# Performance work log

Hardware: AMD Instinct MI355X
Metric: run time of the kernel (lower is better)

The kernel has to match this reference:

```python
import jax, jax.numpy as jnp
import numpy as np

N = 50000   # nodes
E = 800000  # edges (avg degree 16)
D = 64      # in_feat
OUT = 64    # out_feat


def _layernorm(x, gamma, beta, eps=1e-5):
    m = jnp.mean(x, axis=-1, keepdims=True)
    v = jnp.mean((x - m) ** 2, axis=-1, keepdims=True)  # biased var, as torch LayerNorm
    return (x - m) * jax.lax.rsqrt(v + eps) * gamma + beta


def setup_inputs() -> dict:
    key = jax.random.key(0)
    ks = jax.random.split(key, 6)
    s1 = 1.0 / np.sqrt(D)
    s2 = 1.0 / np.sqrt(2 * D)
    return {
        "x": jax.random.normal(ks[0], (N, D), dtype=jnp.float32),
        "edge_index": jax.random.randint(ks[1], (2, E), 0, N, dtype=jnp.int64),
        "W1a": jax.random.normal(ks[2], (D, D), dtype=jnp.float32) * s1,
        "W1b": jax.random.normal(ks[3], (D, D), dtype=jnp.float32) * s1,
        "gamma1": jnp.ones((D,), jnp.float32),
        "beta1": jnp.zeros((D,), jnp.float32),
        "w": jnp.ones((D,), jnp.float32),
        "gamma2": jnp.ones((D,), jnp.float32),
        "beta2": jnp.zeros((D,), jnp.float32),
        "W2a": jax.random.normal(ks[4], (D, 2 * D), dtype=jnp.float32) * s2,
        "W2b": jax.random.normal(ks[5], (OUT, D), dtype=jnp.float32) * s1,
    }


def reference(x, edge_index, W1a, W1b, gamma1, beta1, w, gamma2, beta2, W2a, W2b):
    row, col = edge_index[0], edge_index[1]
    n = x.shape[0]
    # gather -> MLP1 (two bias-free linears with ReLU)
    msg = x[row]                                        # [E, D]
    msg = jax.nn.relu(msg @ W1a.T) @ W1b.T              # [E, D]
    # scatter_mean over destination nodes
    s = jax.ops.segment_sum(msg, col, num_segments=n)   # [N, D]
    cnt = jax.ops.segment_sum(jnp.ones((col.shape[0],), x.dtype), col, num_segments=n)
    agg = s / jnp.maximum(cnt, 1.0)[:, None]
    agg = _layernorm(agg, gamma1, beta1)
    # repulsion + residual + LayerNorm
    fx = _layernorm(x + (x - agg) * w, gamma2, beta2)
    # concat -> MLP2
    h = jnp.concatenate([fx, agg], axis=1)              # [N, 2D]
    return jax.nn.relu(h @ W2a.T) @ W2b.T               # [N, OUT]
```

## Files before the change

### kernel.cpp

```cpp
#include <hip/hip_runtime.h>
#include <hip/hip_bf16.h>

#define NN 50000
#define NE 800000
#define CAP 48
#define BINS 196
#define P1B 98
#define CHUNK 8164
#define MLPB 768
#define SUPT 782

typedef short v8s __attribute__((ext_vector_type(8)));
typedef float v4f __attribute__((ext_vector_type(4)));
#define MFMA16(a, b, c) __builtin_amdgcn_mfma_f32_16x16x32_bf16(a, b, c, 0, 0, 0)

__device__ __forceinline__ float bfu2f(unsigned short u) {
    union { unsigned int i; float f; } v; v.i = ((unsigned int)u) << 16; return v.f;
}
__device__ __forceinline__ unsigned short f2bf_rne(float f) {
    union { float f; unsigned int i; } v; v.f = f;
    unsigned int x = v.i;
    unsigned int r = x + 0x7fffu + ((x >> 16) & 1u);
    return (unsigned short)(r >> 16);
}
__device__ __forceinline__ v8s fragf32(const float* p) {
    float4 u = ((const float4*)p)[0];
    float4 v = ((const float4*)p)[1];
    v8s r;
    r[0] = (short)f2bf_rne(u.x); r[1] = (short)f2bf_rne(u.y);
    r[2] = (short)f2bf_rne(u.z); r[3] = (short)f2bf_rne(u.w);
    r[4] = (short)f2bf_rne(v.x); r[5] = (short)f2bf_rne(v.y);
    r[6] = (short)f2bf_rne(v.z); r[7] = (short)f2bf_rne(v.w);
    return r;
}
__device__ __forceinline__ v8s fragbf(const unsigned short* p) {
    union { uint4 u; v8s s; } t; t.u = *((const uint4*)p); return t.s;
}
__device__ __forceinline__ v4f vzero() { v4f z; z[0]=0.f; z[1]=0.f; z[2]=0.f; z[3]=0.f; return z; }

__global__ __launch_bounds__(256) void p1fat_k(const int* __restrict__ ei,
                                               const float* __restrict__ x,
                                               const float* __restrict__ W1a,
                                               const float* __restrict__ W1b,
                                               unsigned int* __restrict__ chunkbuf,
                                               unsigned short* __restrict__ histT,
                                               unsigned short* __restrict__ y) {
    __shared__ unsigned int smem[8616];
    int t = threadIdx.x;
    if (blockIdx.x < P1B) {
        unsigned int* hcnt = smem;
        unsigned int* scan = smem + BINS;
        unsigned int* data = smem + BINS + 256;
        int p = blockIdx.x;
        int e0 = p * CHUNK;
        int e1 = e0 + CHUNK; if (e1 > NE) e1 = NE;
        int ne = e1 - e0;
        bool i64 = ((ei[1] | ei[3] | ei[5] | ei[7]) == 0);
        for (int i = t; i < BINS; i += 256) hcnt[i] = 0;
        __syncthreads();
        unsigned int packed[32];
#pragma unroll
        for (int i = 0; i < 32; ++i) {
            int e = e0 + t + 256 * i;
            unsigned int pk = 0xFFFFFFFFu;
            if (e < e1) {
                int col = i64 ? ei[2 * (NE + e)] : ei[NE + e];
                int row = i64 ? ei[2 * e]        : ei[e];
                pk = ((unsigned int)col << 16) | (unsigned int)row;
                atomicAdd(&hcnt[col >> 8], 1u);
            }
            packed[i] = pk;
        }
        __syncthreads();
        scan[t] = (t < BINS) ? hcnt[t] : 0;
        __syncthreads();
        for (int off = 1; off < 256; off <<= 1) {
            unsigned int a = (t >= off) ? scan[t - off] : 0;
            __syncthreads();
            scan[t] += a;
            __syncthreads();
        }
        if (t < BINS) {
            unsigned int st = scan[t] - hcnt[t];
            scan[t] = st;
            hcnt[t] = st;
        }
        __syncthreads();
#pragma unroll
        for (int i = 0; i < 32; ++i) {
            unsigned int pk = packed[i];
            if (pk != 0xFFFFFFFFu) {
                unsigned int pos = atomicAdd(&hcnt[pk >> 24], 1u);
                data[pos] = pk;
            }
        }
        __syncthreads();
        unsigned int* cb = chunkbuf + (size_t)p * CHUNK;
        for (int i = t; i < ne; i += 256) cb[i] = data[i];
        for (int i = t; i < BINS; i += 256)
            histT[i * P1B + p] = (unsigned short)scan[i];
        return;
    }
    unsigned short* wa  = (unsigned short*)smem;
    unsigned short* wb  = wa + 64 * 72;
    unsigned short* h1s = wb + 64 * 72;
    for (int i = t; i < 64 * 64; i += 256) {
        int r = i >> 6, c = i & 63;
        wa[r * 72 + c] = f2bf_rne(W1a[i]);
        wb[r * 72 + c] = f2bf_rne(W1b[i]);
    }
    __syncthreads();
    int w = t >> 6, l = t & 63;
    int lm = l & 15, lq = l >> 4;
    for (int st = blockIdx.x - P1B; st < SUPT; st += MLPB) {
        int nb = st * 64;
        int arow = nb + w * 16 + lm;
        int arc = arow < NN ? arow : NN - 1;
        const float* xr = x + (size_t)arc * 64;
        v8s a0 = fragf32(xr + lq * 8);
        v8s a1 = fragf32(xr + 32 + lq * 8);
        v4f acc[4];
#pragma unroll
        for (int jt = 0; jt < 4; ++jt) acc[jt] = vzero();
#pragma unroll
        for (int jt = 0; jt < 4; ++jt) {
            const unsigned short* wr = &wa[(jt * 16 + lm) * 72];
            acc[jt] = MFMA16(a0, fragbf(wr + lq * 8), acc[jt]);
            acc[jt] = MFMA16(a1, fragbf(wr + 32 + lq * 8), acc[jt]);
        }
#pragma unroll
        for (int jt = 0; jt < 4; ++jt)
#pragma unroll
            for (int r = 0; r < 4; ++r)
                h1s[(w * 16 + lq * 4 + r) * 72 + jt * 16 + lm] = f2bf_rne(fmaxf(acc[jt][r], 0.0f));
        __syncthreads();
        v8s c0 = fragbf(&h1s[(w * 16 + lm) * 72 + lq * 8]);
        v8s c1 = fragbf(&h1s[(w * 16 + lm) * 72 + 32 + lq * 8]);
        v4f acc2[4];
#pragma unroll
        for (int jt = 0; jt < 4; ++jt) acc2[jt] = vzero();
#pragma unroll
        for (int jt = 0; jt < 4; ++jt) {
            const unsigned short* wr = &wb[(jt * 16 + lm) * 72];
            acc2[jt] = MFMA16(c0, fragbf(wr + lq * 8), acc2[jt]);
            acc2[jt] = MFMA16(c1, fragbf(wr + 32 + lq * 8), acc2[jt]);
        }
#pragma unroll
        for (int jt = 0; jt < 4; ++jt)
#pragma unroll
            for (int r = 0; r < 4; ++r) {
                int n = nb + w * 16 + lq * 4 + r;
                if (n < NN) y[(size_t)n * 64 + jt * 16 + lm] = f2bf_rne(acc2[jt][r]);
            }
        __syncthreads();
    }
}

__global__ __launch_bounds__(256) void p2_k(const unsigned int* __restrict__ chunkbuf,
                                            const unsigned short* __restrict__ histT,
                                            unsigned short* __restrict__ bucket1,
                                            int* __restrict__ cnt) {
    __shared__ unsigned int cl[256];
    __shared__ unsigned short dl[256 * CAP];
    __shared__ unsigned int scan[128];
    __shared__ unsigned short sstart[P1B];
    __shared__ unsigned short base[P1B];
    int t = threadIdx.x;
    int b = blockIdx.x;
    int c0 = b << 8;
    for (int i = t; i < 256; i += 256) cl[i] = 0;
    for (int i = t; i < 256 * CAP / 2; i += 256) ((unsigned int*)dl)[i] = 0;
    unsigned int len = 0;
    if (t < P1B) {
        unsigned int st = histT[b * P1B + t];
        int ne = NE - t * CHUNK; if (ne > CHUNK) ne = CHUNK;
        unsigned int en = (b == BINS - 1) ? (unsigned int)ne : histT[(b + 1) * P1B + t];
        len = en - st;
        sstart[t] = (unsigned short)st;
    }
    if (t < 128) scan[t] = (t < P1B) ? len : 0;
    __syncthreads();
    for (int off = 1; off < 128; off <<= 1) {
        unsigned int a = (t < 128 && t >= off) ? scan[t - off] : 0;
        __syncthreads();
        if (t < 128) scan[t] += a;
        __syncthreads();
    }
    if (t < P1B) base[t] = (unsigned short)(scan[t] - len);
    __syncthreads();
    int tot = (int)scan[P1B - 1];
    for (int k = t; k < tot; k += 256) {
        int lo = 0, hi = P1B - 1;
#pragma unroll
        for (int it = 0; it < 7; ++it) {
            int mid = (lo + hi + 1) >> 1;
            if ((int)base[mid] <= k) lo = mid; else hi = mid - 1;
        }
        int idx = (int)sstart[lo] + (k - (int)base[lo]);
        unsigned int d = chunkbuf[(size_t)lo * CHUNK + idx];
        int c = (int)(d >> 16) - c0;
        unsigned int slot = atomicAdd(&cl[c], 1u);
        if (slot < CAP) dl[c * CAP + slot] = (unsigned short)(d & 0xffffu);
    }
    __syncthreads();
    for (int i = t; i < 256; i += 256)
        if (c0 + i < NN) cnt[c0 + i] = (int)cl[i];
    uint4* dst = (uint4*)(bucket1 + (size_t)c0 * CAP);
    const uint4* src = (const uint4*)dl;
    for (int i = t; i < 256 * CAP / 8; i += 256) dst[i] = src[i];
}

__device__ __forceinline__ float wsum64(float v) {
#pragma unroll
    for (int o = 32; o > 0; o >>= 1) v += __shfl_xor(v, o, 64);
    return v;
}
__device__ __forceinline__ void ln_store(float s0, float s1, int tdeg, int n, int p, int j, int f0,
                                         const float* __restrict__ x,
                                         const float* __restrict__ g1, const float* __restrict__ b1,
                                         const float* __restrict__ wrep,
                                         const float* __restrict__ g2, const float* __restrict__ b2,
                                         unsigned short* __restrict__ h) {
    float inv = 1.0f / (float)(tdeg > 1 ? tdeg : 1);
    float a0 = s0 * inv, a1 = s1 * inv;
    float m = wsum64(a0 + a1) * (1.0f / 128.0f);
    float d0 = a0 - m, d1 = a1 - m;
    float var = wsum64(d0 * d0 + d1 * d1) * (1.0f / 128.0f);
    float r = rsqrtf(var + 1e-5f);
    float2 g1v = *(const float2*)(g1 + f0);
    float2 b1v = *(const float2*)(b1 + f0);
    a0 = d0 * r * g1v.x + b1v.x;
    a1 = d1 * r * g1v.y + b1v.y;
    float2 xv = *(const float2*)(x + (size_t)n * 64 + f0);
    float2 wv = *(const float2*)(wrep + f0);
    float t0 = xv.x + (xv.x - a0) * wv.x;
    float t1 = xv.y + (xv.y - a1) * wv.y;
    float m2 = wsum64(t0 + t1) * (1.0f / 128.0f);
    float e0 = t0 - m2, e1 = t1 - m2;
    float var2 = wsum64(e0 * e0 + e1 * e1) * (1.0f / 128.0f);
    float r2 = rsqrtf(var2 + 1e-5f);
    float2 g2v = *(const float2*)(g2 + f0);
    float2 b2v = *(const float2*)(b2 + f0);
    float fx0 = e0 * r2 * g2v.x + b2v.x;
    float fx1 = e1 * r2 * g2v.y + b2v.y;
    unsigned* hw = (unsigned*)(h + (size_t)n * 128);
    if (p == 0) hw[j]      = (unsigned)f2bf_rne(fx0) | ((unsigned)f2bf_rne(fx1) << 16);
    else        hw[32 + j] = (unsigned)f2bf_rne(a0)  | ((unsigned)f2bf_rne(a1)  << 16);
}
__global__ __launch_bounds__(256) void gathernorm_k(const int* __restrict__ cnt,
                                                    const unsigned short* __restrict__ bucket1,
                                                    const unsigned short* __restrict__ y,
                                                    const float* __restrict__ x,
                                                    const float* __restrict__ g1, const float* __restrict__ b1,
                                                    const float* __restrict__ wrep,
                                                    const float* __restrict__ g2, const float* __restrict__ b2,
                                                    unsigned short* __restrict__ h) {
    int n0 = blockIdx.x * 8 + (threadIdx.x >> 6) * 2;
    if (n0 >= NN) return;
    int n1 = n0 + 1;
    int n1c = n1 < NN ? n1 : n0;
    int l = threadIdx.x & 63;
    int p = l >> 5;
    int j = l & 31;
    int f0 = 2 * j;
    int dA = cnt[n0], dB = cnt[n1c];
    int eA = dA < CAP ? dA : CAP;
    int eB = dB < CAP ? dB : CAP;
    const uint4* bpA = (const uint4*)(bucket1 + (size_t)n0 * CAP);
    const uint4* bpB = (const uint4*)(bucket1 + (size_t)n1c * CAP);
    uint4 qA[6], qB[6];
#pragma unroll
    for (int i = 0; i < 6; ++i) { qA[i] = bpA[i]; qB[i] = bpB[i]; }
    float sA0 = 0.f, sA1 = 0.f, sB0 = 0.f, sB1 = 0.f;
#pragma unroll
    for (int c = 0; c < 6; ++c) {
        bool cA = c * 8 < eA, cB = c * 8 < eB;
        if (cA | cB) {
            unsigned wA[4] = { qA[c].x, qA[c].y, qA[c].z, qA[c].w };
            unsigned wB[4] = { qB[c].x, qB[c].y, qB[c].z, qB[c].w };
#pragma unroll
            for (int i = 0; i < 4; ++i) {
                int e = c * 8 + 2 * i + p;
                int idA = (int)((wA[i] >> (p * 16)) & 0xffffu);
                int idB = (int)((wB[i] >> (p * 16)) & 0xffffu);
                unsigned uA = *(const unsigned*)(y + (size_t)idA * 64 + f0);
                unsigned uB = *(const unsigned*)(y + (size_t)idB * 64 + f0);
                bool okA = cA && e < eA, okB = cB && e < eB;
                sA0 += okA ? bfu2f((unsigned short)(uA & 0xffffu)) : 0.0f;
                sA1 += okA ? bfu2f((unsigned short)(uA >> 16)) : 0.0f;
                sB0 += okB ? bfu2f((unsigned short)(uB & 0xffffu)) : 0.0f;
                sB1 += okB ? bfu2f((unsigned short)(uB >> 16)) : 0.0f;
            }
        }
    }
    sA0 += __shfl_xor(sA0, 32, 64);
    sA1 += __shfl_xor(sA1, 32, 64);
    sB0 += __shfl_xor(sB0, 32, 64);
    sB1 += __shfl_xor(sB1, 32, 64);
    ln_store(sA0, sA1, dA, n0, p, j, f0, x, g1, b1, wrep, g2, b2, h);
    if (n1 < NN)
        ln_store(sB0, sB1, dB, n1, p, j, f0, x, g1, b1, wrep, g2, b2, h);
}

__global__ __launch_bounds__(256) void mlp2_k(const unsigned short* hin,
                                              const float* __restrict__ W2a,
                                              const float* __restrict__ W2b,
                                              float* out) {
    __shared__ unsigned short sm2[64 * 136 + 64 * 72 + 64 * 72];
    unsigned short* wa2 = sm2;
    unsigned short* wb2 = wa2 + 64 * 136;
    unsigned short* t2s = wb2 + 64 * 72;
    int t = threadIdx.x;
    for (int i = t; i < 64 * 128; i += 256) {
        int r = i >> 7, c = i & 127;
        wa2[r * 136 + c] = f2bf_rne(W2a[i]);
    }
    for (int i = t; i < 64 * 64; i += 256) {
        int r = i >> 6, c = i & 63;
        wb2[r * 72 + c] = f2bf_rne(W2b[i]);
    }
    __syncthreads();
    int w = t >> 6, l = t & 63;
    int lm = l & 15, lq = l >> 4;
    for (int st = blockIdx.x; st < SUPT; st += MLPB) {
        int nb = st * 64;
        int arow = nb + w * 16 + lm;
        int arc = arow < NN ? arow : NN - 1;
        const unsigned short* fr = hin + (size_t)arc * 128;
        v8s a0 = fragbf(fr + lq * 8);
        v8s a1 = fragbf(fr + 32 + lq * 8);
        v8s a2 = fragbf(fr + 64 + lq * 8);
        v8s a3 = fragbf(fr + 96 + lq * 8);
        v4f acc[4];
#pragma unroll
        for (int jt = 0; jt < 4; ++jt) acc[jt] = vzero();
#pragma unroll
        for (int jt = 0; jt < 4; ++jt) {
            const unsigned short* wr = &wa2[(jt * 16 + lm) * 136];
            acc[jt] = MFMA16(a0, fragbf(wr + lq * 8), acc[jt]);
            acc[jt] = MFMA16(a1, fragbf(wr + 32 + lq * 8), acc[jt]);
            acc[jt] = MFMA16(a2, fragbf(wr + 64 + lq * 8), acc[jt]);
            acc[jt] = MFMA16(a3, fragbf(wr + 96 + lq * 8), acc[jt]);
        }
#pragma unroll
        for (int jt = 0; jt < 4; ++jt)
#pragma unroll
            for (int r = 0; r < 4; ++r)
                t2s[(w * 16 + lq * 4 + r) * 72 + jt * 16 + lm] = f2bf_rne(fmaxf(acc[jt][r], 0.0f));
        __syncthreads();
        v8s c0 = fragbf(&t2s[(w * 16 + lm) * 72 + lq * 8]);
        v8s c1 = fragbf(&t2s[(w * 16 + lm) * 72 + 32 + lq * 8]);
        v4f acc2[4];
#pragma unroll
        for (int jt = 0; jt < 4; ++jt) acc2[jt] = vzero();
#pragma unroll
        for (int jt = 0; jt < 4; ++jt) {
            const unsigned short* wr = &wb2[(jt * 16 + lm) * 72];
            acc2[jt] = MFMA16(c0, fragbf(wr + lq * 8), acc2[jt]);
            acc2[jt] = MFMA16(c1, fragbf(wr + 32 + lq * 8), acc2[jt]);
        }
#pragma unroll
        for (int jt = 0; jt < 4; ++jt)
#pragma unroll
            for (int r = 0; r < 4; ++r) {
                int n = nb + w * 16 + lq * 4 + r;
                if (n < NN) out[(size_t)n * 64 + jt * 16 + lm] = acc2[jt][r];
            }
        __syncthreads();
    }
}

extern "C" void kernel_launch(void* const* d_in, const int* in_sizes, int n_in,
                              void* d_out, int out_size, void* d_ws, size_t ws_size,
                              hipStream_t stream) {
    const float* x   = (const float*)d_in[0];
    const int*   ei  = (const int*)d_in[1];
    const float* W1a = (const float*)d_in[2];
    const float* W1b = (const float*)d_in[3];
    const float* g1  = (const float*)d_in[4];
    const float* b1  = (const float*)d_in[5];
    const float* w   = (const float*)d_in[6];
    const float* g2  = (const float*)d_in[7];
    const float* b2  = (const float*)d_in[8];
    const float* W2a = (const float*)d_in[9];
    const float* W2b = (const float*)d_in[10];

    char* ws = (char*)d_ws;
    unsigned short* y        = (unsigned short*)(ws + 0);
    unsigned int*   chunkbuf = (unsigned int*)(ws + 6400000);
    unsigned short* histT    = (unsigned short*)(ws + 9600288);
    unsigned short* bucket1  = (unsigned short*)(ws + 9638720);
    int*            cnt      = (int*)(ws + 14455616);

    p1fat_k<<<P1B + MLPB, 256, 0, stream>>>(ei, x, W1a, W1b, chunkbuf, histT, y);
    p2_k<<<BINS, 256, 0, stream>>>(chunkbuf, histT, bucket1, cnt);
    gathernorm_k<<<(NN + 7) / 8, 256, 0, stream>>>(cnt, bucket1, y, x,
                                                   g1, b1, w, g2, b2, (unsigned short*)d_out);
    mlp2_k<<<MLPB, 256, 0, stream>>>((const unsigned short*)d_out, W2a, W2b, (float*)d_out);
    (void)in_sizes; (void)n_in; (void)out_size; (void)ws_size;
}
```

Before: 151.9 us.

## Fuse gather-normalize and MLP2 into one kernel staging h in LDS

Merges the gather/LayerNorm kernel with the MLP2 kernel so that each block builds a 64-node tile of the concatenated features in shared memory and runs the MFMA MLP on it directly. This removes the bf16 round trip of h through global memory and one kernel launch. In exchange, the gather phase now runs at the MLP grid size (768 blocks) with each wave handling 16 nodes serially, which lowers the memory-level parallelism available to the irregular gathers. It also adds extra LDS use and a block barrier per tile.

```diff
diff --git a/kernel.cpp b/kernel.cpp
--- a/kernel.cpp
+++ b/kernel.cpp
@@ -220,7 +220,7 @@
                                          const float* __restrict__ g1, const float* __restrict__ b1,
                                          const float* __restrict__ wrep,
                                          const float* __restrict__ g2, const float* __restrict__ b2,
-                                         unsigned short* __restrict__ h) {
+                                         unsigned* __restrict__ hw) {
     float inv = 1.0f / (float)(tdeg > 1 ? tdeg : 1);
     float a0 = s0 * inv, a1 = s1 * inv;
     float m = wsum64(a0 + a1) * (1.0f / 128.0f);
@@ -243,73 +243,24 @@
     float2 b2v = *(const float2*)(b2 + f0);
     float fx0 = e0 * r2 * g2v.x + b2v.x;
     float fx1 = e1 * r2 * g2v.y + b2v.y;
-    unsigned* hw = (unsigned*)(h + (size_t)n * 128);
     if (p == 0) hw[j]      = (unsigned)f2bf_rne(fx0) | ((unsigned)f2bf_rne(fx1) << 16);
     else        hw[32 + j] = (unsigned)f2bf_rne(a0)  | ((unsigned)f2bf_rne(a1)  << 16);
 }
-__global__ __launch_bounds__(256) void gathernorm_k(const int* __restrict__ cnt,
-                                                    const unsigned short* __restrict__ bucket1,
-                                                    const unsigned short* __restrict__ y,
-                                                    const float* __restrict__ x,
-                                                    const float* __restrict__ g1, const float* __restrict__ b1,
-                                                    const float* __restrict__ wrep,
-                                                    const float* __restrict__ g2, const float* __restrict__ b2,
-                                                    unsigned short* __restrict__ h) {
-    int n0 = blockIdx.x * 8 + (threadIdx.x >> 6) * 2;
-    if (n0 >= NN) return;
-    int n1 = n0 + 1;
-    int n1c = n1 < NN ? n1 : n0;
-    int l = threadIdx.x & 63;
-    int p = l >> 5;
-    int j = l & 31;
-    int f0 = 2 * j;
-    int dA = cnt[n0], dB = cnt[n1c];
-    int eA = dA < CAP ? dA : CAP;
-    int eB = dB < CAP ? dB : CAP;
-    const uint4* bpA = (const uint4*)(bucket1 + (size_t)n0 * CAP);
-    const uint4* bpB = (const uint4*)(bucket1 + (size_t)n1c * CAP);
-    uint4 qA[6], qB[6];
-#pragma unroll
-    for (int i = 0; i < 6; ++i) { qA[i] = bpA[i]; qB[i] = bpB[i]; }
-    float sA0 = 0.f, sA1 = 0.f, sB0 = 0.f, sB1 = 0.f;
-#pragma unroll
-    for (int c = 0; c < 6; ++c) {
-        bool cA = c * 8 < eA, cB = c * 8 < eB;
-        if (cA | cB) {
-            unsigned wA[4] = { qA[c].x, qA[c].y, qA[c].z, qA[c].w };
-            unsigned wB[4] = { qB[c].x, qB[c].y, qB[c].z, qB[c].w };
-#pragma unroll
-            for (int i = 0; i < 4; ++i) {
-                int e = c * 8 + 2 * i + p;
-                int idA = (int)((wA[i] >> (p * 16)) & 0xffffu);
-                int idB = (int)((wB[i] >> (p * 16)) & 0xffffu);
-                unsigned uA = *(const unsigned*)(y + (size_t)idA * 64 + f0);
-                unsigned uB = *(const unsigned*)(y + (size_t)idB * 64 + f0);
-                bool okA = cA && e < eA, okB = cB && e < eB;
-                sA0 += okA ? bfu2f((unsigned short)(uA & 0xffffu)) : 0.0f;
-                sA1 += okA ? bfu2f((unsigned short)(uA >> 16)) : 0.0f;
-                sB0 += okB ? bfu2f((unsigned short)(uB & 0xffffu)) : 0.0f;
-                sB1 += okB ? bfu2f((unsigned short)(uB >> 16)) : 0.0f;
-            }
-        }
-    }
-    sA0 += __shfl_xor(sA0, 32, 64);
-    sA1 += __shfl_xor(sA1, 32, 64);
-    sB0 += __shfl_xor(sB0, 32, 64);
-    sB1 += __shfl_xor(sB1, 32, 64);
-    ln_store(sA0, sA1, dA, n0, p, j, f0, x, g1, b1, wrep, g2, b2, h);
-    if (n1 < NN)
-        ln_store(sB0, sB1, dB, n1, p, j, f0, x, g1, b1, wrep, g2, b2, h);
-}
-
-__global__ __launch_bounds__(256) void mlp2_k(const unsigned short* hin,
-                                              const float* __restrict__ W2a,
-                                              const float* __restrict__ W2b,
-                                              float* out) {
-    __shared__ unsigned short sm2[64 * 136 + 64 * 72 + 64 * 72];
-    unsigned short* wa2 = sm2;
-    unsigned short* wb2 = wa2 + 64 * 136;
-    unsigned short* t2s = wb2 + 64 * 72;
+
+__global__ __launch_bounds__(256) void gn2_k(const int* __restrict__ cnt,
+                                             const unsigned short* __restrict__ bucket1,
+                                             const unsigned short* __restrict__ y,
+                                             const float* __restrict__ x,
+                                             const float* __restrict__ g1, const float* __restrict__ b1,
+                                             const float* __restrict__ wrep,
+                                             const float* __restrict__ g2, const float* __restrict__ b2,
+                                             const float* __restrict__ W2a,
+                                             const float* __restrict__ W2b,
+                                             float* __restrict__ out) {
+    __shared__ unsigned short wa2[64 * 136];
+    __shared__ unsigned short wb2[64 * 72];
+    __shared__ unsigned short hs[64 * 136];
+    __shared__ unsigned short t2s[64 * 72];
     int t = threadIdx.x;
     for (int i = t; i < 64 * 128; i += 256) {
         int r = i >> 7, c = i & 127;
@@ -321,12 +272,58 @@
     }
     __syncthreads();
     int w = t >> 6, l = t & 63;
+    int p = l >> 5;
+    int j = l & 31;
+    int f0 = 2 * j;
     int lm = l & 15, lq = l >> 4;
     for (int st = blockIdx.x; st < SUPT; st += MLPB) {
         int nb = st * 64;
-        int arow = nb + w * 16 + lm;
-        int arc = arow < NN ? arow : NN - 1;
-        const unsigned short* fr = hin + (size_t)arc * 128;
+        for (int it = 0; it < 8; ++it) {
+            int n0 = nb + w * 16 + it * 2;
+            int n1 = n0 + 1;
+            int n0c = n0 < NN ? n0 : NN - 1;
+            int n1c = n1 < NN ? n1 : NN - 1;
+            int dA = cnt[n0c], dB = cnt[n1c];
+            int eA = dA < CAP ? dA : CAP;
+            int eB = dB < CAP ? dB : CAP;
+            const uint4* bpA = (const uint4*)(bucket1 + (size_t)n0c * CAP);
+            const uint4* bpB = (const uint4*)(bucket1 + (size_t)n1c * CAP);
+            uint4 qA[6], qB[6];
+#pragma unroll
+            for (int i = 0; i < 6; ++i) { qA[i] = bpA[i]; qB[i] = bpB[i]; }
+            float sA0 = 0.f, sA1 = 0.f, sB0 = 0.f, sB1 = 0.f;
+#pragma unroll
+            for (int c = 0; c < 6; ++c) {
+                bool cA = c * 8 < eA, cB = c * 8 < eB;
+                if (cA | cB) {
+                    unsigned wA[4] = { qA[c].x, qA[c].y, qA[c].z, qA[c].w };
+                    unsigned wB[4] = { qB[c].x, qB[c].y, qB[c].z, qB[c].w };
+#pragma unroll
+                    for (int i = 0; i < 4; ++i) {
+                        int e = c * 8 + 2 * i + p;
+                        int idA = (int)((wA[i] >> (p * 16)) & 0xffffu);
+                        int idB = (int)((wB[i] >> (p * 16)) & 0xffffu);
+                        unsigned uA = *(const unsigned*)(y + (size_t)idA * 64 + f0);
+                        unsigned uB = *(const unsigned*)(y + (size_t)idB * 64 + f0);
+                        bool okA = cA && e < eA, okB = cB && e < eB;
+                        sA0 += okA ? bfu2f((unsigned short)(uA & 0xffffu)) : 0.0f;
+                        sA1 += okA ? bfu2f((unsigned short)(uA >> 16)) : 0.0f;
+                        sB0 += okB ? bfu2f((unsigned short)(uB & 0xffffu)) : 0.0f;
+                        sB1 += okB ? bfu2f((unsigned short)(uB >> 16)) : 0.0f;
+                    }
+                }
+            }
+            sA0 += __shfl_xor(sA0, 32, 64);
+            sA1 += __shfl_xor(sA1, 32, 64);
+            sB0 += __shfl_xor(sB0, 32, 64);
+            sB1 += __shfl_xor(sB1, 32, 64);
+            ln_store(sA0, sA1, dA, n0c, p, j, f0, x, g1, b1, wrep, g2, b2,
+                     (unsigned*)(hs + (size_t)(n0 - nb) * 136));
+            ln_store(sB0, sB1, dB, n1c, p, j, f0, x, g1, b1, wrep, g2, b2,
+                     (unsigned*)(hs + (size_t)(n1 - nb) * 136));
+        }
+        __syncthreads();
+        const unsigned short* fr = hs + (w * 16 + lm) * 136;
         v8s a0 = fragbf(fr + lq * 8);
         v8s a1 = fragbf(fr + 32 + lq * 8);
         v8s a2 = fragbf(fr + 64 + lq * 8);
@@ -394,8 +391,7 @@
 
     p1fat_k<<<P1B + MLPB, 256, 0, stream>>>(ei, x, W1a, W1b, chunkbuf, histT, y);
     p2_k<<<BINS, 256, 0, stream>>>(chunkbuf, histT, bucket1, cnt);
-    gathernorm_k<<<(NN + 7) / 8, 256, 0, stream>>>(cnt, bucket1, y, x,
-                                                   g1, b1, w, g2, b2, (unsigned short*)d_out);
-    mlp2_k<<<MLPB, 256, 0, stream>>>((const unsigned short*)d_out, W2a, W2b, (float*)d_out);
+    gn2_k<<<MLPB, 256, 0, stream>>>(cnt, bucket1, y, x, g1, b1, w, g2, b2,
+                                    W2a, W2b, (float*)d_out);
     (void)in_sizes; (void)n_in; (void)out_size; (void)ws_size;
 }
```

Result: slower. 187.9 us (+23.7%).

## Replace two-pass counting-sort bucketing with direct global atomic bucket insertion

Applied to the files above, without the earlier changes.

Drops the chunked histogram/scan/scatter pass and the second per-bin compaction kernel. Edges are now binned by destination straight into fixed-capacity global buckets, using a global atomicAdd on a per-node counter that a small new kernel zeroes first. This removes a kernel launch and the chunkbuf round trip through memory. In exchange it adds 800k contended global atomics and scattered 2-byte stores. Row order within a bucket now depends on scheduling, which can change float summation order.

```diff
diff --git a/kernel.cpp b/kernel.cpp
--- a/kernel.cpp
+++ b/kernel.cpp
@@ -4,9 +4,7 @@
 #define NN 50000
 #define NE 800000
 #define CAP 48
-#define BINS 196
-#define P1B 98
-#define CHUNK 8164
+#define SCB 1024
 #define MLPB 768
 #define SUPT 782
 
@@ -38,67 +36,29 @@
 }
 __device__ __forceinline__ v4f vzero() { v4f z; z[0]=0.f; z[1]=0.f; z[2]=0.f; z[3]=0.f; return z; }
 
+__global__ __launch_bounds__(256) void zcnt_k(int* __restrict__ cnt) {
+    int i = blockIdx.x * 256 + threadIdx.x;
+    if (i < NN) cnt[i] = 0;
+}
+
 __global__ __launch_bounds__(256) void p1fat_k(const int* __restrict__ ei,
                                                const float* __restrict__ x,
                                                const float* __restrict__ W1a,
                                                const float* __restrict__ W1b,
-                                               unsigned int* __restrict__ chunkbuf,
-                                               unsigned short* __restrict__ histT,
+                                               unsigned short* __restrict__ bucket1,
+                                               int* __restrict__ cnt,
                                                unsigned short* __restrict__ y) {
-    __shared__ unsigned int smem[8616];
+    __shared__ unsigned int smem[6912];
     int t = threadIdx.x;
-    if (blockIdx.x < P1B) {
-        unsigned int* hcnt = smem;
-        unsigned int* scan = smem + BINS;
-        unsigned int* data = smem + BINS + 256;
-        int p = blockIdx.x;
-        int e0 = p * CHUNK;
-        int e1 = e0 + CHUNK; if (e1 > NE) e1 = NE;
-        int ne = e1 - e0;
+    if (blockIdx.x < SCB) {
         bool i64 = ((ei[1] | ei[3] | ei[5] | ei[7]) == 0);
-        for (int i = t; i < BINS; i += 256) hcnt[i] = 0;
-        __syncthreads();
-        unsigned int packed[32];
-#pragma unroll
-        for (int i = 0; i < 32; ++i) {
-            int e = e0 + t + 256 * i;
-            unsigned int pk = 0xFFFFFFFFu;
-            if (e < e1) {
-                int col = i64 ? ei[2 * (NE + e)] : ei[NE + e];
-                int row = i64 ? ei[2 * e]        : ei[e];
-                pk = ((unsigned int)col << 16) | (unsigned int)row;
-                atomicAdd(&hcnt[col >> 8], 1u);
-            }
-            packed[i] = pk;
-        }
-        __syncthreads();
-        scan[t] = (t < BINS) ? hcnt[t] : 0;
-        __syncthreads();
-        for (int off = 1; off < 256; off <<= 1) {
-            unsigned int a = (t >= off) ? scan[t - off] : 0;
-            __syncthreads();
-            scan[t] += a;
-            __syncthreads();
-        }
-        if (t < BINS) {
-            unsigned int st = scan[t] - hcnt[t];
-            scan[t] = st;
-            hcnt[t] = st;
-        }
-        __syncthreads();
-#pragma unroll
-        for (int i = 0; i < 32; ++i) {
-            unsigned int pk = packed[i];
-            if (pk != 0xFFFFFFFFu) {
-                unsigned int pos = atomicAdd(&hcnt[pk >> 24], 1u);
-                data[pos] = pk;
-            }
-        }
-        __syncthreads();
-        unsigned int* cb = chunkbuf + (size_t)p * CHUNK;
-        for (int i = t; i < ne; i += 256) cb[i] = data[i];
-        for (int i = t; i < BINS; i += 256)
-            histT[i * P1B + p] = (unsigned short)scan[i];
+        for (int e = blockIdx.x * 256 + t; e < NE; e += SCB * 256) {
+            int col = i64 ? ei[2 * (NE + e)] : ei[NE + e];
+            int row = i64 ? ei[2 * e]        : ei[e];
+            int slot = atomicAdd(&cnt[col], 1);
+            if (slot < CAP)
+                bucket1[(size_t)col * CAP + slot] = (unsigned short)row;
+        }
         return;
     }
     unsigned short* wa  = (unsigned short*)smem;
@@ -112,7 +72,7 @@
     __syncthreads();
     int w = t >> 6, l = t & 63;
     int lm = l & 15, lq = l >> 4;
-    for (int st = blockIdx.x - P1B; st < SUPT; st += MLPB) {
+    for (int st = blockIdx.x - SCB; st < SUPT; st += MLPB) {
         int nb = st * 64;
         int arow = nb + w * 16 + lm;
         int arc = arow < NN ? arow : NN - 1;
@@ -154,60 +114,6 @@
             }
         __syncthreads();
     }
-}
-
-__global__ __launch_bounds__(256) void p2_k(const unsigned int* __restrict__ chunkbuf,
-                                            const unsigned short* __restrict__ histT,
-                                            unsigned short* __restrict__ bucket1,
-                                            int* __restrict__ cnt) {
-    __shared__ unsigned int cl[256];
-    __shared__ unsigned short dl[256 * CAP];
-    __shared__ unsigned int scan[128];
-    __shared__ unsigned short sstart[P1B];
-    __shared__ unsigned short base[P1B];
-    int t = threadIdx.x;
-    int b = blockIdx.x;
-    int c0 = b << 8;
-    for (int i = t; i < 256; i += 256) cl[i] = 0;
-    for (int i = t; i < 256 * CAP / 2; i += 256) ((unsigned int*)dl)[i] = 0;
-    unsigned int len = 0;
-    if (t < P1B) {
-        unsigned int st = histT[b * P1B + t];
-        int ne = NE - t * CHUNK; if (ne > CHUNK) ne = CHUNK;
-        unsigned int en = (b == BINS - 1) ? (unsigned int)ne : histT[(b + 1) * P1B + t];
-        len = en - st;
-        sstart[t] = (unsigned short)st;
-    }
-    if (t < 128) scan[t] = (t < P1B) ? len : 0;
-    __syncthreads();
-    for (int off = 1; off < 128; off <<= 1) {
-        unsigned int a = (t < 128 && t >= off) ? scan[t - off] : 0;
-        __syncthreads();
-        if (t < 128) scan[t] += a;
-        __syncthreads();
-    }
-    if (t < P1B) base[t] = (unsigned short)(scan[t] - len);
-    __syncthreads();
-    int tot = (int)scan[P1B - 1];
-    for (int k = t; k < tot; k += 256) {
-        int lo = 0, hi = P1B - 1;
-#pragma unroll
-        for (int it = 0; it < 7; ++it) {
-            int mid = (lo + hi + 1) >> 1;
-            if ((int)base[mid] <= k) lo = mid; else hi = mid - 1;
-        }
-        int idx = (int)sstart[lo] + (k - (int)base[lo]);
-        unsigned int d = chunkbuf[(size_t)lo * CHUNK + idx];
-        int c = (int)(d >> 16) - c0;
-        unsigned int slot = atomicAdd(&cl[c], 1u);
-        if (slot < CAP) dl[c * CAP + slot] = (unsigned short)(d & 0xffffu);
-    }
-    __syncthreads();
-    for (int i = t; i < 256; i += 256)
-        if (c0 + i < NN) cnt[c0 + i] = (int)cl[i];
-    uint4* dst = (uint4*)(bucket1 + (size_t)c0 * CAP);
-    const uint4* src = (const uint4*)dl;
-    for (int i = t; i < 256 * CAP / 8; i += 256) dst[i] = src[i];
 }
 
 __device__ __forceinline__ float wsum64(float v) {
@@ -386,14 +292,12 @@
     const float* W2b = (const float*)d_in[10];
 
     char* ws = (char*)d_ws;
-    unsigned short* y        = (unsigned short*)(ws + 0);
-    unsigned int*   chunkbuf = (unsigned int*)(ws + 6400000);
-    unsigned short* histT    = (unsigned short*)(ws + 9600288);
-    unsigned short* bucket1  = (unsigned short*)(ws + 9638720);
-    int*            cnt      = (int*)(ws + 14455616);
-
-    p1fat_k<<<P1B + MLPB, 256, 0, stream>>>(ei, x, W1a, W1b, chunkbuf, histT, y);
-    p2_k<<<BINS, 256, 0, stream>>>(chunkbuf, histT, bucket1, cnt);
+    unsigned short* y       = (unsigned short*)(ws + 0);
+    unsigned short* bucket1 = (unsigned short*)(ws + 6400000);
+    int*            cnt     = (int*)(ws + 11216896);
+
+    zcnt_k<<<(NN + 255) / 256, 256, 0, stream>>>(cnt);
+    p1fat_k<<<SCB + MLPB, 256, 0, stream>>>(ei, x, W1a, W1b, bucket1, cnt, y);
     gathernorm_k<<<(NN + 7) / 8, 256, 0, stream>>>(cnt, bucket1, y, x,
                                                    g1, b1, w, g2, b2, (unsigned short*)d_out);
     mlp2_k<<<MLPB, 256, 0, stream>>>((const unsigned short*)d_out, W2a, W2b, (float*)d_out);
```

Result: slower. 175.7 us (+15.7%).
